# Kernel tuning notes

Measured on AMD Instinct MI355X. Metric: run time of the kernel, lower is better.

The kernel has to match this reference:

```python
import jax, jax.numpy as jnp
import numpy as np
from jax import lax

T, B, C, N, NKV, H = 4, 8, 256, 2048, 2048, 8
EPS = 1e-5
TAU = 2.0
ALPHA = 4.0  # spikingjelly Sigmoid surrogate default
SCALE = 0.125

@jax.custom_vjp
def spike(x):
    return (x >= 0.0).astype(x.dtype)

def _spike_fwd(x):
    return (x >= 0.0).astype(x.dtype), x

def _spike_bwd(x, g):
    s = jax.nn.sigmoid(ALPHA * x)
    return (g * ALPHA * s * (1.0 - s),)

spike.defvjp(_spike_fwd, _spike_bwd)

def lif(x, v_th):
    # x: [T, ...]; multi-step LIF: v += (x - v)/tau, fire at v_th, hard reset to 0 (detach_reset)
    def step(v, xt):
        v = v + (xt - v) / TAU
        s = spike(v - v_th)
        v = v * (1.0 - lax.stop_gradient(s))
        return v, s
    _, s = lax.scan(step, jnp.zeros_like(x[0]), x)
    return s

def bn_apply(x, p):
    # x: [M, C, L]; p: [4, C] = (gamma, beta, running_mean, running_var); inference BN
    g, b, mu, var = p
    inv = g / jnp.sqrt(var + EPS)
    return (x - mu[:, None]) * inv[:, None] + b[:, None]

def repconv(x, w1, p1, w3, w2, p2):
    # x: [M, C, L] -> [M, C, L]
    x = jnp.einsum('oc,mcl->mol', w1, x)  # 1x1 conv
    g, b, mu, var = p1
    inv = g / jnp.sqrt(var + EPS)
    x = (x - mu[:, None]) * inv[:, None] + b[:, None]
    pad = b - mu * inv  # BNAndPadLayer pad values [C]
    pad = jnp.broadcast_to(pad[None, :, None], (x.shape[0], x.shape[1], 1))
    x = jnp.concatenate([pad, x, pad], axis=2)
    # depthwise conv k=3, valid
    x = x[:, :, :-2] * w3[:, 0:1] + x[:, :, 1:-1] * w3[:, 1:2] + x[:, :, 2:] * w3[:, 2:3]
    x = jnp.einsum('oc,mcl->mol', w2, x)  # 1x1 conv
    return bn_apply(x, p2)

def _make_bn(key, n):
    k1, k2, k3, k4 = jax.random.split(key, 4)
    g = jax.random.uniform(k1, (n, C)) * 0.5 + 0.75
    b = jax.random.normal(k2, (n, C)) * 0.1
    mu = jax.random.normal(k3, (n, C)) * 0.1
    var = jax.random.uniform(k4, (n, C)) + 0.5
    return jnp.stack([g, b, mu, var], axis=1).astype(jnp.float32)  # [n, 4, C]

def setup_inputs():
    key = jax.random.key(0)
    ks = jax.random.split(key, 8)
    q = jax.random.normal(ks[0], (T, B, C, N), dtype=jnp.float32)
    k_ = jax.random.normal(ks[1], (T, B, C, NKV), dtype=jnp.float32)
    s1 = 1.0 / np.sqrt(C).astype(np.float32)
    rc_w1 = jax.random.normal(ks[2], (6, C, C), dtype=jnp.float32) * s1
    rc_w3 = jax.random.normal(ks[3], (6, C, 3), dtype=jnp.float32) * 0.3
    rc_w2 = jax.random.normal(ks[4], (6, C, C), dtype=jnp.float32) * s1
    rc_bn1 = _make_bn(ks[5], 6)
    rc_bn2 = _make_bn(ks[6], 6)
    out_bn = _make_bn(ks[7], 6)
    return {"q": q, "k_": k_, "rc_w1": rc_w1, "rc_bn1": rc_bn1, "rc_w3": rc_w3,
            "rc_w2": rc_w2, "rc_bn2": rc_bn2, "out_bn": out_bn}

def reference(q, k_, rc_w1, rc_bn1, rc_w3, rc_w2, rc_bn2, out_bn):
    Tt, Bb, Cc, Nn = q.shape
    hd = Cc // H

    def conv_bn(x, i):  # RepConv(i) followed by BatchNorm1d(i), over flattened (T*B)
        L = x.shape[-1]
        y = x.reshape(Tt * Bb, Cc, L)
        y = repconv(y, rc_w1[i], rc_bn1[i], rc_w3[i], rc_w2[i], rc_bn2[i])
        y = bn_apply(y, out_bn[i])
        return y.reshape(Tt, Bb, Cc, L)

    qf = conv_bn(q, 0)
    kf = conv_bn(conv_bn(k_, 1), 2)
    vf = conv_bn(conv_bn(k_, 3), 4)

    def to_heads(x):  # [T,B,C,L] -> [T,B,H,L,hd]
        L = x.shape[-1]
        return x.transpose(0, 1, 3, 2).reshape(Tt, Bb, L, H, hd).transpose(0, 1, 3, 2, 4)

    qh = to_heads(lif(qf, 1.0))
    kh = to_heads(lif(kf, 1.0))
    vh = to_heads(lif(vf, 1.0))
    kv = jnp.einsum('tbhnd,tbhne->tbhde', kh, vh)          # [T,B,H,hd,hd]
    a = jnp.einsum('tbhmd,tbhde->tbhme', qh, kv) * SCALE   # [T,B,H,N,hd]
    a = a.transpose(0, 1, 2, 4, 3).reshape(Tt, Bb, Cc, Nn)
    a = lif(a, 0.5)  # attn_lif, v_threshold=0.5
    return conv_bn(a, 5)
```

## Files before the change

### kernel.cpp

```cpp
#include <hip/hip_runtime.h>

#define C 256
#define NPOS 2048
#define BB 8
#define TTIME 4
#define PRM_STRIDE 132096
#define FRAG_ELEMS 196608

typedef float f32x4 __attribute__((ext_vector_type(4)));
typedef short short8 __attribute__((ext_vector_type(8)));
typedef unsigned int u32x4 __attribute__((ext_vector_type(4)));

static __device__ __forceinline__ unsigned short f2bf(float f) {
    unsigned int u = __float_as_uint(f);
    return (unsigned short)((u + 0x7FFFu + ((u >> 16) & 1u)) >> 16);
}
static __device__ __forceinline__ float bf2f(unsigned short b) {
    return __uint_as_float(((unsigned int)b) << 16);
}
static __device__ __forceinline__ void split3(float f, unsigned short& h,
                                              unsigned short& m, unsigned short& l) {
    h = f2bf(f);
    float r1 = f - bf2f(h);
    m = f2bf(r1);
    float r2 = r1 - bf2f(m);
    l = f2bf(r2);
}
static __device__ __forceinline__ unsigned long long pack4(const unsigned short* a) {
    return (unsigned long long)a[0] | ((unsigned long long)a[1] << 16)
         | ((unsigned long long)a[2] << 32) | ((unsigned long long)a[3] << 48);
}

__global__ __launch_bounds__(256) void prep_kern(
    const float* __restrict__ w1g, const float* __restrict__ bn1,
    const float* __restrict__ w3g, const float* __restrict__ w2g,
    const float* __restrict__ bn2, const float* __restrict__ bno,
    float* __restrict__ prm)
{
    int i = blockIdx.x;
    int tid = threadIdx.x;
    __shared__ float s1l[C], hcl[C], SGl[C];
    const float* b1 = bn1 + i * 4 * C;
    const float* b2 = bn2 + i * 4 * C;
    const float* bo = bno + i * 4 * C;
    float g1 = b1[tid], be1 = b1[C + tid], mu1 = b1[2 * C + tid], va1 = b1[3 * C + tid];
    float s1 = g1 / sqrtf(va1 + 1e-5f);
    float h1 = be1 - mu1 * s1;
    float g2 = b2[tid], be2 = b2[C + tid], mu2 = b2[2 * C + tid], va2 = b2[3 * C + tid];
    float s2 = g2 / sqrtf(va2 + 1e-5f);
    float h2 = be2 - mu2 * s2;
    float go = bo[tid], beo = bo[C + tid], muo = bo[2 * C + tid], vao = bo[3 * C + tid];
    float so = go / sqrtf(vao + 1e-5f);
    float ho = beo - muo * so;
    float SG = so * s2;
    float SH = so * h2 + ho;
    const float* w3i = w3g + i * C * 3;
    float w3s = w3i[tid * 3 + 0] + w3i[tid * 3 + 1] + w3i[tid * 3 + 2];
    s1l[tid] = s1; hcl[tid] = w3s * h1; SGl[tid] = SG;
    __syncthreads();
    float* prmi = prm + (size_t)i * PRM_STRIDE;
    const float* w1i = w1g + (size_t)i * C * C;
    const float* w2i = w2g + (size_t)i * C * C;
    for (int k = 0; k < C; ++k)
        prmi[tid * C + k] = s1l[k] * w1i[k * C + tid];
    for (int k = 0; k < C; ++k)
        prmi[65536 + tid * C + k] = SGl[k] * w2i[k * C + tid];
    for (int j = 0; j < 3; ++j)
        prmi[131072 + j * C + tid] = w3i[tid * 3 + j];
    float dot = 0.f;
    for (int k = 0; k < C; ++k)
        dot = fmaf(w2i[tid * C + k], hcl[k], dot);
    prmi[131840 + tid] = SG * dot + SH;
}

__global__ __launch_bounds__(256) void prep2_kern(
    const float* __restrict__ prm, unsigned short* __restrict__ frags)
{
    int b = blockIdx.x;
    int i = b >> 1, which = b & 1;
    const float* src = prm + (size_t)i * PRM_STRIDE + which * 65536;
    unsigned short* dst = frags + (size_t)b * FRAG_ELEMS;
    for (int e = threadIdx.x; e < 65536; e += 256) {
        int m = e & 255, k = e >> 8;
        float w = src[k * 256 + m];
        unsigned short h, mi, lo;
        split3(w, h, mi, lo);
        int ks = k >> 5, kin = k & 31;
        int mt = m >> 4;
        int lane = (m & 15) | (((kin >> 3) & 3) << 4);
        int j = kin & 7;
        size_t base = ((size_t)(ks * 16 + mt) * 3) * 64 * 8 + lane * 8 + j;
        dst[base] = h;
        dst[base + 512] = mi;
        dst[base + 1024] = lo;
    }
}

template<int IN_MODE, int OUT_T>
__global__ __launch_bounds__(256, 2) void conv_fused(
    const float* __restrict__ x, const unsigned int* __restrict__ xmask,
    float* __restrict__ y, const unsigned short* __restrict__ fragA,
    const unsigned short* __restrict__ fragB, const float* __restrict__ prmi)
{
    __shared__ __align__(16) char lds[61440];
    const int tid = threadIdx.x;
    const int lane = tid & 63, wv = tid >> 6;
    const int ctile = blockIdx.x & 31;
    const int slice = blockIdx.x >> 5;
    const int l0 = ctile * 64;
    const int lo4 = lane & 15, rg = lane >> 4;
    const int PA[6] = {0, 0, 1, 0, 2, 1};
    const int PB[6] = {0, 1, 0, 2, 0, 1};

    int mt[4];
#pragma unroll
    for (int rt = 0; rt < 4; ++rt) mt[rt] = wv * 2 + (rt & 1) + ((rt >> 1) << 3);

    f32x4 acc1[4][5];
#pragma unroll
    for (int a = 0; a < 4; ++a)
#pragma unroll
        for (int b = 0; b < 5; ++b) acc1[a][b] = (f32x4)0.f;

    const short8* Ab1 = (const short8*)fragA;

#pragma unroll
    for (int p = 0; p < 2; ++p) {
#pragma unroll
        for (int it = 0; it < 5; ++it) {
            int u = it * 256 + tid;
            int col = u % 80;
            int oct = u / 80;
            int gpos = l0 - 8 + col;
            int kq = p * 128 + oct * 8;
            bool ok = (unsigned)gpos < (unsigned)NPOS;
            char* wb = lds + col * 256 + (((oct ^ (col & 7)) & 15) << 4);
            if (IN_MODE == 2) {
                u32x4 hp = (u32x4)0u;
                if (ok) {
                    const unsigned int* mg = xmask + (size_t)slice * C * 64 + (gpos >> 5);
                    int bitp = gpos & 31;
#pragma unroll
                    for (int j2 = 0; j2 < 4; ++j2) {
                        unsigned int b0 = (mg[(kq + 2 * j2) * 64] >> bitp) & 1u;
                        unsigned int b1 = (mg[(kq + 2 * j2 + 1) * 64] >> bitp) & 1u;
                        hp[j2] = (b0 ? 0x3F80u : 0u) | ((b1 ? 0x3F80u : 0u) << 16);
                    }
                }
                *(u32x4*)wb = hp;
            } else {
                float xv[8];
                if (ok) {
                    if (IN_MODE == 0) {
                        const float* xg = x + (size_t)slice * C * NPOS + gpos;
#pragma unroll
                        for (int j = 0; j < 8; ++j)
                            xv[j] = xg[(size_t)(kq + j) * NPOS];
                    } else {
                        const float4* rp = (const float4*)(x + ((size_t)slice * NPOS + gpos) * C + kq);
                        float4 a = rp[0], b = rp[1];
                        xv[0] = a.x; xv[1] = a.y; xv[2] = a.z; xv[3] = a.w;
                        xv[4] = b.x; xv[5] = b.y; xv[6] = b.z; xv[7] = b.w;
                    }
                } else {
#pragma unroll
                    for (int j = 0; j < 8; ++j) xv[j] = 0.f;
                }
                unsigned short h[8], m[8], l[8];
#pragma unroll
                for (int j = 0; j < 8; ++j) split3(xv[j], h[j], m[j], l[j]);
                u32x4 hp, mp, lp;
#pragma unroll
                for (int j2 = 0; j2 < 4; ++j2) {
                    hp[j2] = (unsigned int)h[2 * j2] | ((unsigned int)h[2 * j2 + 1] << 16);
                    mp[j2] = (unsigned int)m[2 * j2] | ((unsigned int)m[2 * j2 + 1] << 16);
                    lp[j2] = (unsigned int)l[2 * j2] | ((unsigned int)l[2 * j2 + 1] << 16);
                }
                *(u32x4*)wb = hp;
                *(u32x4*)(wb + 20480) = mp;
                *(u32x4*)(wb + 40960) = lp;
            }
        }
        __syncthreads();
#pragma unroll
        for (int ksl = 0; ksl < 4; ++ksl) {
            int ks = p * 4 + ksl;
            int oct = ksl * 4 + rg;
            short8 A[4][3];
#pragma unroll
            for (int rt = 0; rt < 4; ++rt)
#pragma unroll
                for (int s = 0; s < 3; ++s)
                    A[rt][s] = Ab1[(size_t)((ks * 16 + mt[rt]) * 3 + s) * 64 + lane];
            int ba[5];
#pragma unroll
            for (int ct = 0; ct < 5; ++ct) {
                int colb = ct * 16 + lo4;
                ba[ct] = colb * 256 + (((oct ^ (colb & 7)) & 15) << 4);
            }
            if (IN_MODE == 2) {
                short8 B[5];
#pragma unroll
                for (int ct = 0; ct < 5; ++ct)
                    B[ct] = *(const short8*)(lds + ba[ct]);
                __builtin_amdgcn_s_setprio(1);
#pragma unroll
                for (int pp = 0; pp < 3; ++pp)
#pragma unroll
                    for (int rt = 0; rt < 4; ++rt)
#pragma unroll
                        for (int ct = 0; ct < 5; ++ct)
                            acc1[rt][ct] = __builtin_amdgcn_mfma_f32_16x16x32_bf16(
                                A[rt][pp], B[ct], acc1[rt][ct], 0, 0, 0);
                __builtin_amdgcn_s_setprio(0);
            } else {
                short8 B[5][3];
#pragma unroll
                for (int ct = 0; ct < 5; ++ct) {
                    B[ct][0] = *(const short8*)(lds + ba[ct]);
                    B[ct][1] = *(const short8*)(lds + 20480 + ba[ct]);
                    B[ct][2] = *(const short8*)(lds + 40960 + ba[ct]);
                }
                __builtin_amdgcn_s_setprio(1);
#pragma unroll
                for (int pp = 0; pp < 6; ++pp)
#pragma unroll
                    for (int rt = 0; rt < 4; ++rt)
#pragma unroll
                        for (int ct = 0; ct < 5; ++ct)
                            acc1[rt][ct] = __builtin_amdgcn_mfma_f32_16x16x32_bf16(
                                A[rt][PA[pp]], B[ct][PB[pp]], acc1[rt][ct], 0, 0, 0);
                __builtin_amdgcn_s_setprio(0);
            }
        }
        __syncthreads();
    }

    const float* w3p = prmi + 131072;
    const short8* Ab2 = (const short8*)fragB;
    f32x4 acc2[4][4];
#pragma unroll
    for (int a = 0; a < 4; ++a)
#pragma unroll
        for (int b = 0; b < 4; ++b) acc2[a][b] = (f32x4)0.f;

#pragma unroll
    for (int tp = 0; tp < 2; ++tp) {
#pragma unroll
        for (int rr = 0; rr < 2; ++rr) {
            const int rt = tp * 2 + rr;
            int RTB = mt[rt] << 4;
            float w3a[4], w3b[4], w3c[4];
#pragma unroll
            for (int r = 0; r < 4; ++r) {
                int m = RTB + rg * 4 + r;
                w3a[r] = w3p[m]; w3b[r] = w3p[256 + m]; w3c[r] = w3p[512 + m];
            }
            int k0 = (RTB & 127) + rg * 4;
#pragma unroll
            for (int ct = 0; ct < 5; ++ct) {
                int sc = ct * 16 + lo4;
                unsigned short th[4], tm_[4], tl_[4];
#pragma unroll
                for (int r = 0; r < 4; ++r) {
                    float cur = acc1[rt][ct][r];
                    float prevv = acc1[rt][ct > 0 ? ct - 1 : 0][r];
                    float nextv = acc1[rt][ct < 4 ? ct + 1 : 4][r];
                    float sL  = __shfl(cur, lane - 1);
                    float sL2 = __shfl(prevv, lane + 15);
                    float sR  = __shfl(cur, lane + 1);
                    float sR2 = __shfl(nextv, lane - 15);
                    float uL = lo4 ? sL : sL2;
                    float uR = (lo4 == 15) ? sR2 : sR;
                    float t = w3a[r] * uL + w3b[r] * cur + w3c[r] * uR;
                    split3(t, th[r], tm_[r], tl_[r]);
                }
                if (sc >= 8 && sc < 72) {
                    int oc = sc - 8;
                    int base = oc * 256 + ((((k0 >> 3) ^ (oc & 7)) & 15) << 4) + (k0 & 7) * 2;
                    *(unsigned long long*)(lds + base) = pack4(th);
                    *(unsigned long long*)(lds + 16384 + base) = pack4(tm_);
                    *(unsigned long long*)(lds + 32768 + base) = pack4(tl_);
                }
            }
        }
        __syncthreads();
#pragma unroll
        for (int ksl = 0; ksl < 4; ++ksl) {
            int ks = tp * 4 + ksl;
            int chunk = ksl * 4 + rg;
            short8 A[4][3];
#pragma unroll
            for (int rt = 0; rt < 4; ++rt)
#pragma unroll
                for (int s = 0; s < 3; ++s)
                    A[rt][s] = Ab2[(size_t)((ks * 16 + mt[rt]) * 3 + s) * 64 + lane];
            short8 B[4][3];
#pragma unroll
            for (int ct = 0; ct < 4; ++ct) {
                int oc = ct * 16 + lo4;
                int ba = oc * 256 + (((chunk ^ (oc & 7)) & 15) << 4);
                B[ct][0] = *(const short8*)(lds + ba);
                B[ct][1] = *(const short8*)(lds + 16384 + ba);
                B[ct][2] = *(const short8*)(lds + 32768 + ba);
            }
            __builtin_amdgcn_s_setprio(1);
#pragma unroll
            for (int pp = 0; pp < 6; ++pp)
#pragma unroll
                for (int rt = 0; rt < 4; ++rt)
#pragma unroll
                    for (int ct = 0; ct < 4; ++ct)
                        acc2[rt][ct] = __builtin_amdgcn_mfma_f32_16x16x32_bf16(
                            A[rt][PA[pp]], B[ct][PB[pp]], acc2[rt][ct], 0, 0, 0);
            __builtin_amdgcn_s_setprio(0);
        }
        if (tp == 0) __syncthreads();
    }

    const float* bs = prmi + 131840;
    float* yS = y + (size_t)slice * NPOS * C;
    if (OUT_T) {
#pragma unroll
        for (int ph = 0; ph < 2; ++ph) {
            __syncthreads();
#pragma unroll
            for (int rt = 0; rt < 4; ++rt) {
                int m0 = (mt[rt] << 4) + rg * 4;
                int chunk = (mt[rt] << 2) + rg;
#pragma unroll
                for (int cc = 0; cc < 2; ++cc) {
                    int ct = ph * 2 + cc;
                    int cl = cc * 16 + lo4;
                    f32x4 o;
#pragma unroll
                    for (int r = 0; r < 4; ++r) o[r] = acc2[rt][ct][r] + bs[m0 + r];
                    *(f32x4*)(lds + cl * 1024 + ((chunk ^ (cl & 7)) << 4)) = o;
                }
            }
            __syncthreads();
#pragma unroll
            for (int i = 0; i < 8; ++i) {
                int u = i * 256 + tid;
                int cl = u >> 6, cchunk = u & 63;
                f32x4 o = *(const f32x4*)(lds + cl * 1024 + ((cchunk ^ (cl & 7)) << 4));
                int pos = l0 + ph * 32 + cl;
                *(f32x4*)(yS + (size_t)pos * C + cchunk * 4) = o;
            }
        }
    } else {
#pragma unroll
        for (int rt = 0; rt < 4; ++rt) {
            int m0 = (mt[rt] << 4) + rg * 4;
#pragma unroll
            for (int ct = 0; ct < 4; ++ct) {
                int pos = l0 + ct * 16 + lo4;
#pragma unroll
                for (int r = 0; r < 4; ++r)
                    yS[(size_t)(m0 + r) * NPOS + pos] = acc2[rt][ct][r] + bs[m0 + r];
            }
        }
    }
}

__global__ __launch_bounds__(256) void lif_kern(
    const float* __restrict__ yT, unsigned int* __restrict__ mask, float vth)
{
    int g = blockIdx.x * 256 + threadIdx.x;
    int ch = g & 255;
    int w = (g >> 8) & 63;
    int b = g >> 14;
    float v[32];
#pragma unroll
    for (int j = 0; j < 32; ++j) v[j] = 0.f;
    for (int t = 0; t < TTIME; ++t) {
        int slice = t * BB + b;
        const float* yr = yT + ((size_t)slice * NPOS + w * 32) * C + ch;
        unsigned int mw = 0;
#pragma unroll
        for (int j = 0; j < 32; ++j) {
            float yy = yr[(size_t)j * C];
            float vn = v[j] + (yy - v[j]) * 0.5f;
            int sp = (vn - vth) >= 0.0f;
            mw |= ((unsigned int)sp) << j;
            v[j] = sp ? 0.f : vn;
        }
        mask[((size_t)slice * C + ch) * 64 + w] = mw;
    }
}

__global__ __launch_bounds__(256) void kv_kern(
    const unsigned int* __restrict__ km_g, const unsigned int* __restrict__ vm_g,
    int* __restrict__ kv_g)
{
    int blk = blockIdx.x;
    int h = blk & 7;
    int tb = blk >> 3;
    __shared__ unsigned int km[32][65], vm[32][65];
    int tid = threadIdx.x;
#pragma unroll
    for (int i = 0; i < 8; ++i) {
        int idx = i * 256 + tid;
        int d = idx >> 6, w = idx & 63;
        size_t rb = ((size_t)tb * C + h * 32 + d) * 64 + w;
        km[d][w] = km_g[rb];
        vm[d][w] = vm_g[rb];
    }
    __syncthreads();
#pragma unroll
    for (int k = 0; k < 4; ++k) {
        int p = k * 256 + tid;
        int d = p >> 5, e = p & 31;
        int s = 0;
#pragma unroll
        for (int w = 0; w < 64; ++w)
            s += __popc(km[d][w] & vm[e][w]);
        kv_g[(size_t)blk * 1024 + p] = s;
    }
}

__global__ __launch_bounds__(256) void attn_kern(
    const unsigned int* __restrict__ qm_g, const int* __restrict__ kv_g,
    unsigned int* __restrict__ amask)
{
    int blk = blockIdx.x;
    int chunk = blk & 7;
    int bh = blk >> 3;
    int h = bh & 7, b = bh >> 3;
    int tid = threadIdx.x;
    __shared__ int kvs[1024];
    __shared__ unsigned int qw[32][8];
    float v[32];
#pragma unroll
    for (int e = 0; e < 32; ++e) v[e] = 0.f;
    for (int t = 0; t < TTIME; ++t) {
        int tb = t * BB + b;
        __syncthreads();
#pragma unroll
        for (int k = 0; k < 4; ++k)
            kvs[k * 256 + tid] = kv_g[((size_t)tb * 8 + h) * 1024 + k * 256 + tid];
        {
            int d = tid >> 3, wi = tid & 7;
            qw[d][wi] = qm_g[((size_t)tb * C + h * 32 + d) * 64 + chunk * 8 + wi];
        }
        __syncthreads();
        int a[32];
#pragma unroll
        for (int e = 0; e < 32; ++e) a[e] = 0;
        int wsel = tid >> 5, bitp = tid & 31;
        for (int d = 0; d < 32; ++d) {
            if ((qw[d][wsel] >> bitp) & 1u) {
                const int* kr = &kvs[d * 32];
#pragma unroll
                for (int e = 0; e < 32; ++e) a[e] += kr[e];
            }
        }
#pragma unroll
        for (int e = 0; e < 32; ++e) {
            float f = (float)a[e] * 0.125f;
            v[e] = v[e] + (f - v[e]) * 0.5f;
            int sp = (v[e] - 0.5f) >= 0.0f;
            unsigned long long bb = __ballot(sp);
            if ((tid & 63) == 0) {
                int ch = h * 32 + e;
                unsigned long long* dst = (unsigned long long*)amask
                    + ((size_t)tb * C + ch) * 32 + chunk * 4 + (tid >> 6);
                *dst = bb;
            }
            if (sp) v[e] = 0.f;
        }
    }
}

extern "C" void kernel_launch(void* const* d_in, const int* in_sizes, int n_in,
                              void* d_out, int out_size, void* d_ws, size_t ws_size,
                              hipStream_t stream) {
    const float* q   = (const float*)d_in[0];
    const float* k_  = (const float*)d_in[1];
    const float* w1g = (const float*)d_in[2];
    const float* bn1 = (const float*)d_in[3];
    const float* w3g = (const float*)d_in[4];
    const float* w2g = (const float*)d_in[5];
    const float* bn2 = (const float*)d_in[6];
    const float* bno = (const float*)d_in[7];

    float* prm = (float*)d_ws;
    unsigned short* frags = (unsigned short*)(prm + 6 * PRM_STRIDE);
    float* bufA = (float*)(frags + 12 * FRAG_ELEMS);
    float* bufB = bufA + 16777216;
    unsigned int* qmask = (unsigned int*)(bufB + 16777216);
    unsigned int* kmask = qmask + 524288;
    unsigned int* vmask = kmask + 524288;
    int* kvb = (int*)(vmask + 524288);
    unsigned int* amask = (unsigned int*)(kvb + 262144);

    prep_kern<<<6, 256, 0, stream>>>(w1g, bn1, w3g, w2g, bn2, bno, prm);
    prep2_kern<<<12, 256, 0, stream>>>(prm, frags);

#define FRAG(i, which) (frags + (size_t)((i) * 2 + (which)) * FRAG_ELEMS)
#define PRMI(i) (prm + (size_t)(i) * PRM_STRIDE)

    conv_fused<0, 1><<<1024, 256, 0, stream>>>(q, nullptr, bufA, FRAG(0, 0), FRAG(0, 1), PRMI(0));
    lif_kern<<<512, 256, 0, stream>>>(bufA, qmask, 1.0f);
    conv_fused<0, 1><<<1024, 256, 0, stream>>>(k_, nullptr, bufA, FRAG(1, 0), FRAG(1, 1), PRMI(1));
    conv_fused<1, 1><<<1024, 256, 0, stream>>>(bufA, nullptr, bufB, FRAG(2, 0), FRAG(2, 1), PRMI(2));
    lif_kern<<<512, 256, 0, stream>>>(bufB, kmask, 1.0f);
    conv_fused<0, 1><<<1024, 256, 0, stream>>>(k_, nullptr, bufA, FRAG(3, 0), FRAG(3, 1), PRMI(3));
    conv_fused<1, 1><<<1024, 256, 0, stream>>>(bufA, nullptr, bufB, FRAG(4, 0), FRAG(4, 1), PRMI(4));
    lif_kern<<<512, 256, 0, stream>>>(bufB, vmask, 1.0f);

    kv_kern<<<256, 256, 0, stream>>>(kmask, vmask, kvb);
    attn_kern<<<512, 256, 0, stream>>>(qmask, kvb, amask);

    conv_fused<2, 0><<<1024, 256, 0, stream>>>(nullptr, amask, (float*)d_out, FRAG(5, 0), FRAG(5, 1), PRMI(5));
}
```

Measured before the change: 810.1 us.

## Software-pipeline conv input staging with register prefetch across K chunks

Splits the first GEMM's K dimension into four 64-wide chunks instead of two 128-wide halves. Global loads for the next chunk are issued into registers before the current chunk's MFMA work, then split to bf16 and written to LDS. This is meant to hide global-load latency behind compute and shrinks the staging LDS footprint, so the total shared allocation drops. The cost is extra registers for the prefetch buffers and more barriers per block.

```diff
diff --git a/kernel.cpp b/kernel.cpp
--- a/kernel.cpp
+++ b/kernel.cpp
@@ -102,7 +102,7 @@
     float* __restrict__ y, const unsigned short* __restrict__ fragA,
     const unsigned short* __restrict__ fragB, const float* __restrict__ prmi)
 {
-    __shared__ __align__(16) char lds[61440];
+    __shared__ __align__(16) char lds[49152];
     const int tid = threadIdx.x;
     const int lane = tid & 63, wv = tid >> 6;
     const int ctile = blockIdx.x & 31;
@@ -124,67 +124,79 @@
 
     const short8* Ab1 = (const short8*)fragA;
 
-#pragma unroll
-    for (int p = 0; p < 2; ++p) {
-#pragma unroll
-        for (int it = 0; it < 5; ++it) {
-            int u = it * 256 + tid;
-            int col = u % 80;
-            int oct = u / 80;
-            int gpos = l0 - 8 + col;
-            int kq = p * 128 + oct * 8;
-            bool ok = (unsigned)gpos < (unsigned)NPOS;
-            char* wb = lds + col * 256 + (((oct ^ (col & 7)) & 15) << 4);
-            if (IN_MODE == 2) {
-                u32x4 hp = (u32x4)0u;
-                if (ok) {
-                    const unsigned int* mg = xmask + (size_t)slice * C * 64 + (gpos >> 5);
-                    int bitp = gpos & 31;
-#pragma unroll
-                    for (int j2 = 0; j2 < 4; ++j2) {
-                        unsigned int b0 = (mg[(kq + 2 * j2) * 64] >> bitp) & 1u;
-                        unsigned int b1 = (mg[(kq + 2 * j2 + 1) * 64] >> bitp) & 1u;
-                        hp[j2] = (b0 ? 0x3F80u : 0u) | ((b1 ? 0x3F80u : 0u) << 16);
-                    }
-                }
-                *(u32x4*)wb = hp;
-            } else {
-                float xv[8];
-                if (ok) {
-                    if (IN_MODE == 0) {
-                        const float* xg = x + (size_t)slice * C * NPOS + gpos;
-#pragma unroll
-                        for (int j = 0; j < 8; ++j)
-                            xv[j] = xg[(size_t)(kq + j) * NPOS];
-                    } else {
-                        const float4* rp = (const float4*)(x + ((size_t)slice * NPOS + gpos) * C + kq);
-                        float4 a = rp[0], b = rp[1];
-                        xv[0] = a.x; xv[1] = a.y; xv[2] = a.z; xv[3] = a.w;
-                        xv[4] = b.x; xv[5] = b.y; xv[6] = b.z; xv[7] = b.w;
-                    }
-                } else {
-#pragma unroll
-                    for (int j = 0; j < 8; ++j) xv[j] = 0.f;
-                }
-                unsigned short h[8], m[8], l[8];
-#pragma unroll
-                for (int j = 0; j < 8; ++j) split3(xv[j], h[j], m[j], l[j]);
-                u32x4 hp, mp, lp;
-#pragma unroll
-                for (int j2 = 0; j2 < 4; ++j2) {
-                    hp[j2] = (unsigned int)h[2 * j2] | ((unsigned int)h[2 * j2 + 1] << 16);
-                    mp[j2] = (unsigned int)m[2 * j2] | ((unsigned int)m[2 * j2 + 1] << 16);
-                    lp[j2] = (unsigned int)l[2 * j2] | ((unsigned int)l[2 * j2 + 1] << 16);
-                }
-                *(u32x4*)wb = hp;
-                *(u32x4*)(wb + 20480) = mp;
-                *(u32x4*)(wb + 40960) = lp;
-            }
-        }
+    float LDf[20];
+    unsigned int LDu[20];
+
+#define ISSUE(sp_)                                                             \
+    {                                                                          \
+        _Pragma("unroll")                                                      \
+        for (int it = 0; it < 5; ++it) {                                       \
+            int u = it * 256 + tid;                                            \
+            int col = u % 80;                                                  \
+            int kq4 = u / 80;                                                  \
+            int gpos = l0 - 8 + col;                                           \
+            bool ok = (unsigned)gpos < (unsigned)NPOS;                         \
+            int k0 = (sp_) * 64 + kq4 * 4;                                     \
+            if (IN_MODE == 2) {                                                \
+                const unsigned int* mg = xmask + (size_t)slice * C * 64 + (gpos >> 5); \
+                _Pragma("unroll")                                              \
+                for (int j = 0; j < 4; ++j)                                    \
+                    LDu[it * 4 + j] = ok ? mg[(k0 + j) * 64] : 0u;             \
+            } else if (IN_MODE == 0) {                                         \
+                const float* xg = x + (size_t)slice * C * NPOS + gpos;         \
+                _Pragma("unroll")                                              \
+                for (int j = 0; j < 4; ++j)                                    \
+                    LDf[it * 4 + j] = ok ? xg[(size_t)(k0 + j) * NPOS] : 0.f;  \
+            } else {                                                           \
+                if (ok) {                                                      \
+                    float4 a4 = *(const float4*)(x + ((size_t)slice * NPOS + gpos) * C + k0); \
+                    LDf[it * 4 + 0] = a4.x; LDf[it * 4 + 1] = a4.y;            \
+                    LDf[it * 4 + 2] = a4.z; LDf[it * 4 + 3] = a4.w;            \
+                } else {                                                       \
+                    _Pragma("unroll")                                          \
+                    for (int j = 0; j < 4; ++j) LDf[it * 4 + j] = 0.f;         \
+                }                                                              \
+            }                                                                  \
+        }                                                                      \
+    }
+
+#define SPLIT(sp_)                                                             \
+    {                                                                          \
+        _Pragma("unroll")                                                      \
+        for (int it = 0; it < 5; ++it) {                                       \
+            int u = it * 256 + tid;                                            \
+            int col = u % 80;                                                  \
+            int kq4 = u / 80;                                                  \
+            int base = col * 128 + ((((kq4 >> 1) ^ (col & 7)) & 7) << 4) + (kq4 & 1) * 8; \
+            if (IN_MODE == 2) {                                                \
+                int gpos = l0 - 8 + col;                                       \
+                int bitp = gpos & 31;                                          \
+                unsigned short th[4];                                          \
+                _Pragma("unroll")                                              \
+                for (int j = 0; j < 4; ++j)                                    \
+                    th[j] = ((LDu[it * 4 + j] >> bitp) & 1u) ? 0x3F80 : 0;     \
+                *(unsigned long long*)(lds + base) = pack4(th);                \
+            } else {                                                           \
+                unsigned short th[4], tm_[4], tl_[4];                          \
+                _Pragma("unroll")                                              \
+                for (int j = 0; j < 4; ++j)                                    \
+                    split3(LDf[it * 4 + j], th[j], tm_[j], tl_[j]);            \
+                *(unsigned long long*)(lds + base) = pack4(th);                \
+                *(unsigned long long*)(lds + 10240 + base) = pack4(tm_);       \
+                *(unsigned long long*)(lds + 20480 + base) = pack4(tl_);       \
+            }                                                                  \
+        }                                                                      \
+    }
+
+    ISSUE(0);
+#pragma unroll
+    for (int sp = 0; sp < 4; ++sp) {
+        SPLIT(sp);
+        if (sp < 3) ISSUE(sp + 1);
         __syncthreads();
 #pragma unroll
-        for (int ksl = 0; ksl < 4; ++ksl) {
-            int ks = p * 4 + ksl;
+        for (int ksl = 0; ksl < 2; ++ksl) {
+            int ks = sp * 2 + ksl;
             int oct = ksl * 4 + rg;
             short8 A[4][3];
 #pragma unroll
@@ -196,7 +208,7 @@
 #pragma unroll
             for (int ct = 0; ct < 5; ++ct) {
                 int colb = ct * 16 + lo4;
-                ba[ct] = colb * 256 + (((oct ^ (colb & 7)) & 15) << 4);
+                ba[ct] = colb * 128 + (((oct ^ (colb & 7)) & 7) << 4);
             }
             if (IN_MODE == 2) {
                 short8 B[5];
@@ -218,8 +230,8 @@
 #pragma unroll
                 for (int ct = 0; ct < 5; ++ct) {
                     B[ct][0] = *(const short8*)(lds + ba[ct]);
-                    B[ct][1] = *(const short8*)(lds + 20480 + ba[ct]);
-                    B[ct][2] = *(const short8*)(lds + 40960 + ba[ct]);
+                    B[ct][1] = *(const short8*)(lds + 10240 + ba[ct]);
+                    B[ct][2] = *(const short8*)(lds + 20480 + ba[ct]);
                 }
                 __builtin_amdgcn_s_setprio(1);
 #pragma unroll
@@ -361,6 +373,8 @@
             }
         }
     }
+#undef ISSUE
+#undef SPLIT
 }
 
 __global__ __launch_bounds__(256) void lif_kern(
```

Measured after the change: 814.4 us. No clear change (+0.5%).
